# Kernel optimization log

Measured on AMD Instinct MI355X. Metric: run time of the kernel, lower is better.

The kernel has to match this reference:

```python
import jax, jax.numpy as jnp
import numpy as np

D_MODEL = 1024
D_FF = 4096
N_EXPERTS = 8
TOP_K = 2

def setup_inputs() -> dict:
    key = jax.random.key(0)
    ks = jax.random.split(key, 8)
    s = 1.0 / np.sqrt(D_MODEL)
    sf = 1.0 / np.sqrt(D_FF)
    return {
        "x": jax.random.normal(ks[0], (4, 1024, D_MODEL), dtype=jnp.float32),
        "W1": jax.random.uniform(ks[1], (N_EXPERTS, D_MODEL, D_FF), jnp.float32, -s, s),
        "b1": jax.random.uniform(ks[2], (N_EXPERTS, D_FF), jnp.float32, -s, s),
        "W2": jax.random.uniform(ks[3], (N_EXPERTS, D_FF, D_MODEL), jnp.float32, -sf, sf),
        "b2": jax.random.uniform(ks[4], (N_EXPERTS, D_MODEL), jnp.float32, -sf, sf),
        "Wg": jax.random.uniform(ks[5], (D_MODEL, N_EXPERTS), jnp.float32, -s, s),
        "bg": jax.random.uniform(ks[6], (N_EXPERTS,), jnp.float32, -s, s),
    }

def reference(x, W1, b1, W2, b2, Wg, bg):
    # gate: [B,S,E]
    logits = jnp.einsum('bsd,de->bse', x, Wg) + bg
    probs = jax.nn.softmax(logits, axis=-1)
    # top-k mask + renormalize (k < n_experts)
    topk_vals, topk_idx = jax.lax.top_k(probs, TOP_K)
    mask = jax.nn.one_hot(topk_idx, N_EXPERTS, dtype=probs.dtype).sum(axis=-2)
    probs = probs * mask
    denom = probs.sum(axis=-1, keepdims=True)
    denom = denom + (denom == 0).astype(probs.dtype)
    probs = probs / denom
    # dense expert compute: all experts on all tokens. h: [B,E,S,d_ff]
    h = jnp.einsum('bsd,edf->besf', x, W1) + b1[None, :, None, :]
    h = jax.nn.gelu(h, approximate=False)
    y = jnp.einsum('besf,efd->besd', h, W2) + b2[None, :, None, :]
    # weighted combine over experts: [B,S,d]
    out = jnp.einsum('bse,besd->bsd', probs, y)
    return out
```

## Files before the change

### kernel.cpp

```cpp
#include <hip/hip_runtime.h>
#include <hip/hip_bf16.h>

#define NTOK   4096
#define DMODEL 1024
#define DFF    4096
#define NEXP   8
#define TOPK   2
#define BM 128
#define BN 128
#define BK 64
#define NSLOT   (NTOK*TOPK)
#define MAXSLOT (NSLOT + NEXP*BM)
#define MAXTILE (MAXSLOT/BM)

typedef __attribute__((ext_vector_type(8))) short bf16x8;
typedef __attribute__((ext_vector_type(8))) unsigned short u16x8;
typedef __attribute__((ext_vector_type(4))) float f32x4;

__device__ __forceinline__ unsigned short f2bf(float f){
    union { float f; unsigned int u; } v; v.f = f;
    unsigned int r = (v.u + 0x7fffu + ((v.u >> 16) & 1u)) >> 16;
    return (unsigned short)r;
}

__device__ __forceinline__ void gload16(const unsigned short* g, unsigned short* l){
    __builtin_amdgcn_global_load_lds(
        (const __attribute__((address_space(1))) void*)g,
        (__attribute__((address_space(3))) void*)l,
        16, 0, 0);
}

__global__ __launch_bounds__(256) void k_transpose_convert2(const float* __restrict__ W1,
                                                            const float* __restrict__ W2,
                                                            unsigned short* __restrict__ W1t,
                                                            unsigned short* __restrict__ W2t)
{
    __shared__ unsigned short tile[64][72];
    int z = blockIdx.z;
    const float* src; unsigned short* dst; int R, C, r0, c0;
    if(z < 8){
        src = W1  + (size_t)z * DMODEL * DFF;
        dst = W1t + (size_t)z * DMODEL * DFF;
        R = DMODEL; C = DFF;
        r0 = blockIdx.y * 64; c0 = blockIdx.x * 64;
    } else {
        src = W2  + (size_t)(z-8) * DFF * DMODEL;
        dst = W2t + (size_t)(z-8) * DFF * DMODEL;
        R = DFF; C = DMODEL;
        r0 = blockIdx.x * 64; c0 = blockIdx.y * 64;
    }
    int t = threadIdx.x;
    int tr = t >> 4;
    int tc = (t & 15) * 4;
    #pragma unroll
    for(int i=0;i<4;i++){
        float4 v = *(const float4*)&src[(size_t)(r0 + tr + i*16)*C + c0 + tc];
        tile[tc+0][tr + i*16] = f2bf(v.x);
        tile[tc+1][tr + i*16] = f2bf(v.y);
        tile[tc+2][tr + i*16] = f2bf(v.z);
        tile[tc+3][tr + i*16] = f2bf(v.w);
    }
    __syncthreads();
    int rr  = t >> 3;
    int cc8 = (t & 7) * 8;
    #pragma unroll
    for(int i=0;i<2;i++){
        u16x8 o = *(const u16x8*)&tile[rr + i*32][cc8];
        *(u16x8*)&dst[(size_t)(c0 + rr + i*32)*R + r0 + cc8] = o;
    }
}

__global__ __launch_bounds__(256) void k_gate(const float* __restrict__ x,
                                              const float* __restrict__ Wg,
                                              const float* __restrict__ bg,
                                              unsigned short* __restrict__ Xb,
                                              int* __restrict__ token_e,
                                              float* __restrict__ token_w,
                                              int* __restrict__ cnt)
{
    int tid = threadIdx.x;
    const float4* xs = (const float4*)x + (size_t)blockIdx.x * 1024;
    ushort4* xd = (ushort4*)Xb + (size_t)blockIdx.x * 1024;
    #pragma unroll
    for(int rep=0;rep<4;rep++){
        float4 v = xs[rep*256 + tid];
        ushort4 o; o.x=f2bf(v.x); o.y=f2bf(v.y); o.z=f2bf(v.z); o.w=f2bf(v.w);
        xd[rep*256 + tid] = o;
    }

    int wid = tid >> 6, lane = tid & 63;
    int t = blockIdx.x * 4 + wid;
    const float* xr = x + (size_t)t * DMODEL;
    float pe[NEXP];
    #pragma unroll
    for(int e=0;e<NEXP;e++) pe[e] = 0.f;
    for(int i=0;i<DMODEL/64;i++){
        int d = i*64 + lane;
        float xv = xr[d];
        const float* wr = Wg + (size_t)d * NEXP;
        #pragma unroll
        for(int e=0;e<NEXP;e++) pe[e] += xv * wr[e];
    }
    #pragma unroll
    for(int off=32; off>0; off>>=1){
        #pragma unroll
        for(int e=0;e<NEXP;e++) pe[e] += __shfl_xor(pe[e], off);
    }
    if(lane == 0){
        float lg[NEXP], mx = -1e30f;
        #pragma unroll
        for(int e=0;e<NEXP;e++){ lg[e] = pe[e] + bg[e]; mx = fmaxf(mx, lg[e]); }
        float pr[NEXP];
        #pragma unroll
        for(int e=0;e<NEXP;e++) pr[e] = expf(lg[e] - mx);
        int e0 = 0; float p0 = pr[0];
        #pragma unroll
        for(int e=1;e<NEXP;e++) if(pr[e] > p0){ p0 = pr[e]; e0 = e; }
        int e1 = -1; float p1 = -1.f;
        #pragma unroll
        for(int e=0;e<NEXP;e++) if(e != e0 && pr[e] > p1){ p1 = pr[e]; e1 = e; }
        float dn = p0 + p1;
        token_e[2*t]   = e0; token_w[2*t]   = p0/dn;
        token_e[2*t+1] = e1; token_w[2*t+1] = p1/dn;
        atomicAdd(&cnt[e0], 1); atomicAdd(&cnt[e1], 1);
    }
}

__global__ __launch_bounds__(256) void k_prefix_scatter(const int* __restrict__ cnt,
                                                        const int* __restrict__ token_e,
                                                        const float* __restrict__ token_w,
                                                        int* __restrict__ tile_e,
                                                        int* __restrict__ tile_row0,
                                                        int* __restrict__ tile_valid,
                                                        int* __restrict__ slot_token,
                                                        float* __restrict__ slot_w)
{
    __shared__ int sb[NEXP], scur[NEXP];
    int tid = threadIdx.x;
    if(tid == 0){
        int off = 0, nt = 0;
        for(int e=0;e<NEXP;e++){
            sb[e] = off; scur[e] = 0;
            int c = cnt[e];
            for(int r=0;r<c;r+=BM){
                tile_e[nt] = e; tile_row0[nt] = off + r;
                tile_valid[nt] = (c - r < BM) ? (c - r) : BM;
                nt++;
            }
            off += ((c + BM - 1)/BM)*BM;
        }
        for(int i=nt;i<MAXTILE;i++){ tile_e[i]=0; tile_row0[i]=0; tile_valid[i]=0; }
    }
    for(int s=tid; s<MAXSLOT; s+=256) slot_token[s] = 0;
    __syncthreads();
    for(int i=tid; i<NSLOT; i+=256){
        int e = token_e[i];
        int s = sb[e] + atomicAdd(&scur[e], 1);
        slot_token[s] = i >> 1;
        slot_w[s] = token_w[i];
    }
}

template<bool GATHER, bool GELU>
__global__ __launch_bounds__(256, 3) void k_gemm(const unsigned short* __restrict__ A,
                                                 const unsigned short* __restrict__ Bw,
                                                 const float* __restrict__ bias,
                                                 const int* __restrict__ tile_e,
                                                 const int* __restrict__ tile_row0,
                                                 const int* __restrict__ tile_valid,
                                                 const int* __restrict__ slot_token,
                                                 const float* __restrict__ slot_w,
                                                 unsigned short* __restrict__ OutH,
                                                 float* __restrict__ outF,
                                                 int K, int N)
{
    int xb = blockIdx.x;
    int tid = (xb & 7) * (MAXTILE/8) + (xb >> 3);
    int valid = tile_valid[tid];
    if(valid == 0) return;
    int e = tile_e[tid];
    int row0 = tile_row0[tid];
    int n0 = blockIdx.y * BN;
    const unsigned short* Be = Bw + (size_t)e * N * K;

    __shared__ unsigned short As[BM*BK];
    __shared__ unsigned short Bs[BN*BK];

    int t = threadIdx.x;
    int lane = t & 63;
    int wid = t >> 6;
    int wr = wid >> 1, wc = wid & 1;

    int srow = t >> 3;
    int csw  = (t & 7) ^ (srow & 7);
    const unsigned short* arow[4];
    const unsigned short* brow[4];
    #pragma unroll
    for(int i=0;i<4;i++){
        int r = i*32 + srow;
        size_t aoff;
        if(GATHER) aoff = (size_t)slot_token[row0 + r] * (size_t)K;
        else       aoff = (size_t)(row0 + r) * (size_t)K;
        arow[i] = A  + aoff + csw*8;
        brow[i] = Be + (size_t)(n0 + r)*K + csw*8;
    }
    unsigned short* alds = As + (size_t)t * 8;
    unsigned short* blds = Bs + (size_t)t * 8;

    f32x4 acc[4][4];
    #pragma unroll
    for(int m=0;m<4;m++)
        #pragma unroll
        for(int n=0;n<4;n++)
            acc[m][n] = (f32x4){0.f,0.f,0.f,0.f};

    int rl = lane & 15;
    int g  = lane >> 4;
    int rx = rl & 7;

    for(int k0=0;k0<K;k0+=BK){
        __syncthreads();
        #pragma unroll
        for(int i=0;i<4;i++){
            gload16(arow[i] + k0, alds + i*2048);
            gload16(brow[i] + k0, blds + i*2048);
        }
        __syncthreads();

        #pragma unroll
        for(int kb=0;kb<2;kb++){
            int sw = ((kb*4 + g) ^ rx) * 8;
            bf16x8 af[4], bfv[4];
            #pragma unroll
            for(int m=0;m<4;m++) af[m]  = *(const bf16x8*)&As[(wr*64 + m*16 + rl)*BK + sw];
            #pragma unroll
            for(int n=0;n<4;n++) bfv[n] = *(const bf16x8*)&Bs[(wc*64 + n*16 + rl)*BK + sw];
            #pragma unroll
            for(int m=0;m<4;m++)
                #pragma unroll
                for(int n=0;n<4;n++)
                    acc[m][n] = __builtin_amdgcn_mfma_f32_16x16x32_bf16(af[m], bfv[n], acc[m][n], 0, 0, 0);
        }
    }

    const float* be = bias + (size_t)e * N;
    #pragma unroll
    for(int m=0;m<4;m++){
        int rb = wr*64 + m*16 + g*4;
        #pragma unroll
        for(int j=0;j<4;j++){
            int r = rb + j;
            if(r >= valid) continue;
            size_t grow = (size_t)(row0 + r);
            if(GELU){
                #pragma unroll
                for(int n=0;n<4;n++){
                    int col = n0 + wc*64 + n*16 + rl;
                    float v = acc[m][n][j] + be[col];
                    v = 0.5f * v * (1.f + erff(v * 0.70710678118654752f));
                    OutH[grow * (size_t)N + col] = f2bf(v);
                }
            } else {
                float wsc = slot_w[grow];
                float* orow = outF + (size_t)slot_token[grow] * DMODEL;
                #pragma unroll
                for(int n=0;n<4;n++){
                    int col = n0 + wc*64 + n*16 + rl;
                    float v = (acc[m][n][j] + be[col]) * wsc;
                    atomicAdd(&orow[col], v);
                }
            }
        }
    }
}

extern "C" void kernel_launch(void* const* d_in, const int* in_sizes, int n_in,
                              void* d_out, int out_size, void* d_ws, size_t ws_size,
                              hipStream_t stream)
{
    const float* x  = (const float*)d_in[0];
    const float* W1 = (const float*)d_in[1];
    const float* b1 = (const float*)d_in[2];
    const float* W2 = (const float*)d_in[3];
    const float* b2 = (const float*)d_in[4];
    const float* Wg = (const float*)d_in[5];
    const float* bg = (const float*)d_in[6];
    float* out = (float*)d_out;

    char* p = (char*)d_ws;
    auto alloc = [&](size_t bytes)->char*{
        char* r = p; p += (bytes + 255) & ~(size_t)255; return r;
    };
    unsigned short* W1t = (unsigned short*)alloc((size_t)NEXP*DFF*DMODEL*2);
    unsigned short* W2t = (unsigned short*)alloc((size_t)NEXP*DMODEL*DFF*2);
    unsigned short* Xb  = (unsigned short*)alloc((size_t)NTOK*DMODEL*2);
    unsigned short* H   = (unsigned short*)alloc((size_t)MAXSLOT*DFF*2);
    int*   slot_token = (int*)alloc(MAXSLOT*4);
    float* slot_w     = (float*)alloc(MAXSLOT*4);
    int*   token_e    = (int*)alloc(NSLOT*4);
    float* token_w    = (float*)alloc(NSLOT*4);
    int*   cnt        = (int*)alloc(32);
    int*   tile_e     = (int*)alloc(MAXTILE*4);
    int*   tile_row0  = (int*)alloc(MAXTILE*4);
    int*   tile_valid = (int*)alloc(MAXTILE*4);
    (void)ws_size; (void)in_sizes; (void)n_in; (void)out_size;

    hipMemsetAsync(cnt, 0, 32, stream);
    hipMemsetAsync(out, 0, (size_t)NTOK*DMODEL*4, stream);
    k_gate<<<NTOK/4, 256, 0, stream>>>(x, Wg, bg, Xb, token_e, token_w, cnt);
    k_transpose_convert2<<<dim3(DFF/64, DMODEL/64, 16), 256, 0, stream>>>(W1, W2, W1t, W2t);
    k_prefix_scatter<<<1, 256, 0, stream>>>(cnt, token_e, token_w,
                                            tile_e, tile_row0, tile_valid,
                                            slot_token, slot_w);
    k_gemm<true, true ><<<dim3(MAXTILE, DFF/BN),    256, 0, stream>>>(
        Xb, W1t, b1, tile_e, tile_row0, tile_valid, slot_token, slot_w, H, nullptr, DMODEL, DFF);
    k_gemm<false,false><<<dim3(MAXTILE, DMODEL/BN), 256, 0, stream>>>(
        H,  W2t, b2, tile_e, tile_row0, tile_valid, slot_token, slot_w, nullptr, out, DFF, DMODEL);
}
```

Measured before the change: 481.1 us.

## Enlarge MoE GEMM tiles to 256x256 with 512 threads and split-K second GEMM

Doubles the GEMM block tile to 256x256 and moves to 512-thread blocks of 8 waves, each wave computing a 128x64 sub-tile. The goal is more operand reuse per LDS load and fewer redundant global loads. The second GEMM is split along K into two halves that accumulate through the existing atomics, with the bias added only by the first half, so the grid keeps enough blocks. The transpose kernel now stages fp32 in a padded LDS tile and converts to bf16 when writing out; the cost is more LDS and more registers per thread, plus coarser padding of each expert's rows to 256.

```diff
diff --git a/kernel.cpp b/kernel.cpp
--- a/kernel.cpp
+++ b/kernel.cpp
@@ -6,8 +6,8 @@
 #define DFF    4096
 #define NEXP   8
 #define TOPK   2
-#define BM 128
-#define BN 128
+#define BM 256
+#define BN 256
 #define BK 64
 #define NSLOT   (NTOK*TOPK)
 #define MAXSLOT (NSLOT + NEXP*BM)
@@ -30,12 +30,14 @@
         16, 0, 0);
 }
 
+#define MFMA16(a,b,c) __builtin_amdgcn_mfma_f32_16x16x32_bf16(a,b,c,0,0,0)
+
 __global__ __launch_bounds__(256) void k_transpose_convert2(const float* __restrict__ W1,
                                                             const float* __restrict__ W2,
                                                             unsigned short* __restrict__ W1t,
                                                             unsigned short* __restrict__ W2t)
 {
-    __shared__ unsigned short tile[64][72];
+    __shared__ float tile[64][65];
     int z = blockIdx.z;
     const float* src; unsigned short* dst; int R, C, r0, c0;
     if(z < 8){
@@ -50,23 +52,26 @@
         r0 = blockIdx.x * 64; c0 = blockIdx.y * 64;
     }
     int t = threadIdx.x;
-    int tr = t >> 4;
-    int tc = (t & 15) * 4;
+    int tr  = t >> 4;
+    int tc4 = (t & 15) * 4;
     #pragma unroll
     for(int i=0;i<4;i++){
-        float4 v = *(const float4*)&src[(size_t)(r0 + tr + i*16)*C + c0 + tc];
-        tile[tc+0][tr + i*16] = f2bf(v.x);
-        tile[tc+1][tr + i*16] = f2bf(v.y);
-        tile[tc+2][tr + i*16] = f2bf(v.z);
-        tile[tc+3][tr + i*16] = f2bf(v.w);
+        float4 v = *(const float4*)&src[(size_t)(r0 + tr + i*16)*C + c0 + tc4];
+        tile[tc4+0][tr + i*16] = v.x;
+        tile[tc4+1][tr + i*16] = v.y;
+        tile[tc4+2][tr + i*16] = v.z;
+        tile[tc4+3][tr + i*16] = v.w;
     }
     __syncthreads();
-    int rr  = t >> 3;
-    int cc8 = (t & 7) * 8;
+    int cr = t >> 3;
+    int rb = (t & 7) * 8;
     #pragma unroll
     for(int i=0;i<2;i++){
-        u16x8 o = *(const u16x8*)&tile[rr + i*32][cc8];
-        *(u16x8*)&dst[(size_t)(c0 + rr + i*32)*R + r0 + cc8] = o;
+        int c = cr + i*32;
+        u16x8 o;
+        #pragma unroll
+        for(int q=0;q<8;q++) o[q] = f2bf(tile[c][rb + q]);
+        *(u16x8*)&dst[(size_t)(c0 + c)*R + r0 + rb] = o;
     }
 }
 
@@ -162,7 +167,7 @@
 }
 
 template<bool GATHER, bool GELU>
-__global__ __launch_bounds__(256, 3) void k_gemm(const unsigned short* __restrict__ A,
+__global__ __launch_bounds__(512, 2) void k_gemm(const unsigned short* __restrict__ A,
                                                  const unsigned short* __restrict__ Bw,
                                                  const float* __restrict__ bias,
                                                  const int* __restrict__ tile_e,
@@ -172,7 +177,7 @@
                                                  const float* __restrict__ slot_w,
                                                  unsigned short* __restrict__ OutH,
                                                  float* __restrict__ outF,
-                                                 int K, int N)
+                                                 int lda, int N, int klen)
 {
     int xb = blockIdx.x;
     int tid = (xb & 7) * (MAXTILE/8) + (xb >> 3);
@@ -181,7 +186,8 @@
     int e = tile_e[tid];
     int row0 = tile_row0[tid];
     int n0 = blockIdx.y * BN;
-    const unsigned short* Be = Bw + (size_t)e * N * K;
+    int kbase = blockIdx.z * klen;
+    const unsigned short* Be = Bw + (size_t)e * N * lda;
 
     __shared__ unsigned short As[BM*BK];
     __shared__ unsigned short Bs[BN*BK];
@@ -189,7 +195,7 @@
     int t = threadIdx.x;
     int lane = t & 63;
     int wid = t >> 6;
-    int wr = wid >> 1, wc = wid & 1;
+    int wm = wid >> 2, wn = wid & 3;
 
     int srow = t >> 3;
     int csw  = (t & 7) ^ (srow & 7);
@@ -197,19 +203,19 @@
     const unsigned short* brow[4];
     #pragma unroll
     for(int i=0;i<4;i++){
-        int r = i*32 + srow;
+        int r = i*64 + srow;
         size_t aoff;
-        if(GATHER) aoff = (size_t)slot_token[row0 + r] * (size_t)K;
-        else       aoff = (size_t)(row0 + r) * (size_t)K;
-        arow[i] = A  + aoff + csw*8;
-        brow[i] = Be + (size_t)(n0 + r)*K + csw*8;
+        if(GATHER) aoff = (size_t)slot_token[row0 + r] * (size_t)lda;
+        else       aoff = (size_t)(row0 + r) * (size_t)lda;
+        arow[i] = A  + aoff + kbase + csw*8;
+        brow[i] = Be + (size_t)(n0 + r)*lda + kbase + csw*8;
     }
     unsigned short* alds = As + (size_t)t * 8;
     unsigned short* blds = Bs + (size_t)t * 8;
 
-    f32x4 acc[4][4];
-    #pragma unroll
-    for(int m=0;m<4;m++)
+    f32x4 acc[8][4];
+    #pragma unroll
+    for(int m=0;m<8;m++)
         #pragma unroll
         for(int n=0;n<4;n++)
             acc[m][n] = (f32x4){0.f,0.f,0.f,0.f};
@@ -218,35 +224,39 @@
     int g  = lane >> 4;
     int rx = rl & 7;
 
-    for(int k0=0;k0<K;k0+=BK){
+    for(int k0=0;k0<klen;k0+=BK){
         __syncthreads();
         #pragma unroll
         for(int i=0;i<4;i++){
-            gload16(arow[i] + k0, alds + i*2048);
-            gload16(brow[i] + k0, blds + i*2048);
+            gload16(arow[i] + k0, alds + i*4096);
+            gload16(brow[i] + k0, blds + i*4096);
         }
         __syncthreads();
 
         #pragma unroll
         for(int kb=0;kb<2;kb++){
             int sw = ((kb*4 + g) ^ rx) * 8;
-            bf16x8 af[4], bfv[4];
+            bf16x8 bfv[4];
             #pragma unroll
-            for(int m=0;m<4;m++) af[m]  = *(const bf16x8*)&As[(wr*64 + m*16 + rl)*BK + sw];
+            for(int n=0;n<4;n++) bfv[n] = *(const bf16x8*)&Bs[(wn*64 + n*16 + rl)*BK + sw];
             #pragma unroll
-            for(int n=0;n<4;n++) bfv[n] = *(const bf16x8*)&Bs[(wc*64 + n*16 + rl)*BK + sw];
-            #pragma unroll
-            for(int m=0;m<4;m++)
+            for(int mh=0;mh<2;mh++){
+                bf16x8 af[4];
                 #pragma unroll
-                for(int n=0;n<4;n++)
-                    acc[m][n] = __builtin_amdgcn_mfma_f32_16x16x32_bf16(af[m], bfv[n], acc[m][n], 0, 0, 0);
+                for(int m=0;m<4;m++) af[m] = *(const bf16x8*)&As[(wm*128 + mh*64 + m*16 + rl)*BK + sw];
+                #pragma unroll
+                for(int m=0;m<4;m++)
+                    #pragma unroll
+                    for(int n=0;n<4;n++)
+                        acc[mh*4+m][n] = MFMA16(af[m], bfv[n], acc[mh*4+m][n]);
+            }
         }
     }
 
     const float* be = bias + (size_t)e * N;
     #pragma unroll
-    for(int m=0;m<4;m++){
-        int rb = wr*64 + m*16 + g*4;
+    for(int mi=0;mi<8;mi++){
+        int rb = wm*128 + mi*16 + g*4;
         #pragma unroll
         for(int j=0;j<4;j++){
             int r = rb + j;
@@ -255,8 +265,8 @@
             if(GELU){
                 #pragma unroll
                 for(int n=0;n<4;n++){
-                    int col = n0 + wc*64 + n*16 + rl;
-                    float v = acc[m][n][j] + be[col];
+                    int col = n0 + wn*64 + n*16 + rl;
+                    float v = acc[mi][n][j] + be[col];
                     v = 0.5f * v * (1.f + erff(v * 0.70710678118654752f));
                     OutH[grow * (size_t)N + col] = f2bf(v);
                 }
@@ -265,8 +275,9 @@
                 float* orow = outF + (size_t)slot_token[grow] * DMODEL;
                 #pragma unroll
                 for(int n=0;n<4;n++){
-                    int col = n0 + wc*64 + n*16 + rl;
-                    float v = (acc[m][n][j] + be[col]) * wsc;
+                    int col = n0 + wn*64 + n*16 + rl;
+                    float bterm = (kbase == 0) ? be[col] : 0.f;
+                    float v = (acc[mi][n][j] + bterm) * wsc;
                     atomicAdd(&orow[col], v);
                 }
             }
@@ -312,8 +323,10 @@
     k_prefix_scatter<<<1, 256, 0, stream>>>(cnt, token_e, token_w,
                                             tile_e, tile_row0, tile_valid,
                                             slot_token, slot_w);
-    k_gemm<true, true ><<<dim3(MAXTILE, DFF/BN),    256, 0, stream>>>(
-        Xb, W1t, b1, tile_e, tile_row0, tile_valid, slot_token, slot_w, H, nullptr, DMODEL, DFF);
-    k_gemm<false,false><<<dim3(MAXTILE, DMODEL/BN), 256, 0, stream>>>(
-        H,  W2t, b2, tile_e, tile_row0, tile_valid, slot_token, slot_w, nullptr, out, DFF, DMODEL);
-}
+    k_gemm<true, true ><<<dim3(MAXTILE, DFF/BN, 1),    512, 0, stream>>>(
+        Xb, W1t, b1, tile_e, tile_row0, tile_valid, slot_token, slot_w, H, nullptr,
+        DMODEL, DFF, DMODEL);
+    k_gemm<false,false><<<dim3(MAXTILE, DMODEL/BN, 2), 512, 0, stream>>>(
+        H,  W2t, b2, tile_e, tile_row0, tile_valid, slot_token, slot_w, nullptr, out,
+        DFF, DMODEL, DFF/2);
+}
```

Result: slower. 673.9 us (+40.1%).
